# Kernel optimization log

Measured on AMD Instinct MI355X. Metric: run time of the kernel, lower is better.

The kernel has to match this reference:

```python
import jax, jax.numpy as jnp
from jax import lax
import numpy as np

C = 64
K = 3  # kernel_size
PAD = K // 2


def setup_inputs() -> dict:
    key = jax.random.key(0)
    k1, k2, k3, k4, k5 = jax.random.split(key, 5)
    B, N, H, W = 2, 16, 96, 96
    x = jax.random.normal(k1, (B, C, N, H, W), dtype=jnp.float32)
    # offset conv: Conv2d(C, 2K, kernel=(1,K)) -> 1D conv weight (2K, C, K)
    w_off = jax.random.normal(k2, (2 * K, C, K), dtype=jnp.float32) * 0.05
    b_off = jax.random.normal(k3, (2 * K,), dtype=jnp.float32) * 0.05
    # deform conv: DeformConv2d(C, C, kernel=(1,K)) -> weight (C, C, K)
    w_def = jax.random.normal(k4, (C, C, K), dtype=jnp.float32) * (1.0 / np.sqrt(C * K))
    b_def = jax.random.normal(k5, (C,), dtype=jnp.float32) * 0.01
    return {"x": x, "w_off": w_off, "b_off": b_off, "w_def": w_def, "b_def": b_def}


def _deform_fuse(x, w_off, b_off, w_def, b_def):
    B, Cc, N, H, W = x.shape
    M = B * H * W
    # (B,C,N,H,W) -> (B,H,W,C,N) -> (M, C, N); the 'width' axis is the focus axis N
    xm = jnp.transpose(x, (0, 3, 4, 1, 2)).reshape(M, Cc, N)

    # offset-predicting 1D conv over N, padding K//2 (same)
    offsets = lax.conv_general_dilated(
        xm, w_off, window_strides=(1,), padding=[(PAD, PAD)],
        dimension_numbers=("NCH", "OIH", "NCH"),
    ) + b_off[None, :, None]  # (M, 2K, N)
    # torchvision ordering: per kernel tap j, channel 2j = dy, 2j+1 = dx
    off_y = offsets[:, 0::2]  # (M, K, N)
    off_x = offsets[:, 1::2]  # (M, K, N)

    # base sampling positions along the (width=N) axis: n - pad + j
    pos = (jnp.arange(N, dtype=x.dtype)[None, :] - PAD
           + jnp.arange(K, dtype=x.dtype)[:, None])  # (K, N)
    px = pos[None] + off_x                            # (M, K, N)
    x0 = jnp.floor(px)
    fx = px - x0                                      # fractional part
    x0i = x0.astype(jnp.int32)
    x1i = x0i + 1
    v0 = ((x0i >= 0) & (x0i < N)).astype(x.dtype)
    v1 = ((x1i >= 0) & (x1i < N)).astype(x.dtype)
    c0 = jnp.clip(x0i, 0, N - 1)
    c1 = jnp.clip(x1i, 0, N - 1)

    # gather along N per row: (C,N) indexed by (K,N) -> (C,K,N)
    gather = jax.vmap(lambda xr, idx: xr[:, idx])
    g0 = gather(xm, c0) * (v0 * (1.0 - fx))[:, None]   # (M, C, K, N)
    g1 = gather(xm, c1) * (v1 * fx)[:, None]
    # height dim is size 1: bilinear weight along y collapses to relu(1-|dy|)
    wy = jnp.maximum(jnp.array(0.0, x.dtype), 1.0 - jnp.abs(off_y))[:, None]  # (M,1,K,N)
    val = (g0 + g1) * wy                               # (M, C, K, N)

    out = jnp.einsum("ock,mckn->mon", w_def, val) + b_def[None, :, None]  # (M, C, N)
    out = out.reshape(B, H, W, Cc, N)
    return jnp.transpose(out, (0, 3, 4, 1, 2))         # (B, C, N, H, W)


def reference(x, w_off, b_off, w_def, b_def):
    return _deform_fuse(x, w_off, b_off, w_def, b_def)
```

## Files before the change

### kernel.cpp

```cpp
#include <hip/hip_runtime.h>
#include <stdint.h>


typedef __attribute__((ext_vector_type(8))) short short8;
typedef __attribute__((ext_vector_type(4))) float f32x4;

#define XT_OFF   0
#define XST_OFF  20480
#define PB       36864
#define A0_OFF   (PB)
#define A1_OFF   (PB + 1536)
#define R0_OFF   (PB + 3072)
#define OFFS_OFF (PB + 4608)
#define LDS_BYTES (PB + 7680)

__device__ __forceinline__ short f2bf(float f) {
  union { float f; uint32_t u; } v; v.f = f;
  uint32_t r = (v.u + 0x7FFFu + ((v.u >> 16) & 1u)) >> 16;
  return (short)r;
}
__device__ __forceinline__ float bf2f(short s) {
  union { uint32_t u; float f; } v; v.u = ((uint32_t)(uint16_t)s) << 16; return v.f;
}

__global__ __launch_bounds__(256) void prep_kernel(
    const float* __restrict__ w_off, const float* __restrict__ w_def, short8* __restrict__ ws)
{
  int gid = blockIdx.x * 256 + threadIdx.x;
  if (gid < 1536) {
    int mt = gid / 384, ks = (gid % 384) >> 6, ll = gid & 63;
    int m = mt * 16 + (ll & 15), rgq = ll >> 4;
    short8 v;
    #pragma unroll
    for (int jj = 0; jj < 8; ++jj) {
      int kk = ks * 32 + rgq * 8 + jj;
      int c = kk & 63, k3 = kk >> 6;
      v[jj] = f2bf(w_def[m * 192 + c * 3 + k3]);
    }
    ws[gid] = v;
  } else if (gid < 1920) {
    int q = gid - 1536;
    int ks = q >> 6, ll = q & 63;
    int m = ll & 15, rgq = ll >> 4;
    short8 v;
    #pragma unroll
    for (int jj = 0; jj < 8; ++jj) {
      int kk = ks * 32 + rgq * 8 + jj;
      int c = kk & 63, k3 = kk >> 6;
      v[jj] = (m < 6) ? f2bf(w_off[m * 192 + c * 3 + k3]) : (short)0;
    }
    ws[gid] = v;
  }
}

__global__ __launch_bounds__(256, 3) void deform_main(
    const float* __restrict__ x, const float* __restrict__ b_off,
    const float* __restrict__ b_def, const short8* __restrict__ wfr,
    float* __restrict__ out)
{
  extern __shared__ char smem[];
  const int t = threadIdx.x, wv = t >> 6, l = t & 63, col = l & 15, rg = l >> 4;
  const int tn = blockIdx.x;
  const int wt = tn % 12, bh = tn / 12;
  const int h = bh % 96, b = bh / 96, w0 = wt * 8;
  const float* xb = x + (size_t)b * 9437184 + h * 96 + w0;

  uint16_t* xst = (uint16_t*)(smem + XST_OFF);
  #pragma unroll
  for (int i = 0; i < 8; ++i) {
    int r = (t >> 1) + i * 128, half = t & 1;
    float4 v = *(const float4*)(xb + (size_t)r * 9216 + half * 4);
    uint32_t p0 = (uint32_t)(uint16_t)f2bf(v.x) | ((uint32_t)(uint16_t)f2bf(v.y) << 16);
    uint32_t p1 = (uint32_t)(uint16_t)f2bf(v.z) | ((uint32_t)(uint16_t)f2bf(v.w) << 16);
    uint2 pk; pk.x = p0; pk.y = p1;
    *(uint2*)(xst + r * 8 + half * 4) = pk;
  }
  __syncthreads();

  #pragma unroll
  for (int i = 0; i < 4; ++i) {
    int item = t + 256 * i;
    int pos = item & 127, cg = item >> 7;
    short8 v;
    #pragma unroll
    for (int jj = 0; jj < 8; ++jj) v[jj] = (short)xst[(cg * 8 + jj) * 128 + pos];
    *(short8*)(smem + XT_OFF + pos * 160 + cg * 16) = v;
  }
  __syncthreads();

  float* offs = (float*)(smem + OFFS_OFF);
  {
    f32x4 cacc[2] = {{0.f,0.f,0.f,0.f},{0.f,0.f,0.f,0.f}};
    const short8 zero = {0,0,0,0,0,0,0,0};
    for (int ks = 0; ks < 6; ++ks) {
      short8 av = wfr[1536 + ks * 64 + l];
      int k3 = ks >> 1;
      #pragma unroll
      for (int nt2 = 0; nt2 < 2; ++nt2) {
        int pos = (wv * 2 + nt2) * 16 + col;
        int n = pos >> 3, w = pos & 7;
        int row = n + k3 - 1;
        bool valid = (row >= 0) && (row < 16);
        int rcl = min(max(row, 0), 15);
        short8 bv = *(short8*)(smem + XT_OFF + (rcl * 8 + w) * 160 + rg * 16 + (ks & 1) * 64);
        bv = valid ? bv : zero;
        cacc[nt2] = __builtin_amdgcn_mfma_f32_16x16x32_bf16(av, bv, cacc[nt2], 0, 0, 0);
      }
    }
    #pragma unroll
    for (int nt2 = 0; nt2 < 2; ++nt2) {
      int pos = (wv * 2 + nt2) * 16 + col;
      #pragma unroll
      for (int r = 0; r < 4; ++r) {
        int rowo = rg * 4 + r;
        if (rowo < 6) offs[rowo * 128 + pos] = cacc[nt2][r];
      }
    }
  }
  __syncthreads();

  float* A0 = (float*)(smem + A0_OFF);
  float* A1 = (float*)(smem + A1_OFF);
  int*   R0 = (int*)(smem + R0_OFF);
  for (int it = t; it < 384; it += 256) {
    int k = it >> 7, pos = it & 127;
    int n = pos >> 3, w = pos & 7;
    float oy = offs[(2 * k) * 128 + pos] + b_off[2 * k];
    float ox = offs[(2 * k + 1) * 128 + pos] + b_off[2 * k + 1];
    float px = (float)(n - 1 + k) + ox;
    float x0f = floorf(px);
    float fx = px - x0f;
    int x0 = (int)x0f;
    float wy = fmaxf(0.f, 1.f - fabsf(oy));
    float wt1v = fx * wy;
    float wt0v = wy - wt1v;
    float a0, a1; int r0;
    if (x0 >= 0 && x0 < 15)  { r0 = x0; a0 = wt0v; a1 = wt1v; }
    else if (x0 == 15)       { r0 = 14; a0 = 0.f;  a1 = wt0v; }
    else if (x0 == -1)       { r0 = 0;  a0 = wt1v; a1 = 0.f;  }
    else                     { r0 = 0;  a0 = 0.f;  a1 = 0.f;  }
    A0[it] = a0; A1[it] = a1;
    R0[it] = (r0 * 8 + w) * 160;
  }
  __syncthreads();

  f32x4 acc[4][2];
  #pragma unroll
  for (int mt = 0; mt < 4; ++mt) {
    float4 bd = *(const float4*)(b_def + mt * 16 + rg * 4);
    #pragma unroll
    for (int nt2 = 0; nt2 < 2; ++nt2) {
      acc[mt][nt2][0] = bd.x; acc[mt][nt2][1] = bd.y;
      acc[mt][nt2][2] = bd.z; acc[mt][nt2][3] = bd.w;
    }
  }
  #pragma unroll 1
  for (int k3 = 0; k3 < 3; ++k3) {
    float a0v[2], a1v[2]; int rb[2];
    #pragma unroll
    for (int nt2 = 0; nt2 < 2; ++nt2) {
      int idx = k3 * 128 + (wv * 2 + nt2) * 16 + col;
      a0v[nt2] = A0[idx]; a1v[nt2] = A1[idx]; rb[nt2] = R0[idx];
    }
    #pragma unroll
    for (int ks2 = 0; ks2 < 2; ++ks2) {
      int ks = k3 * 2 + ks2;
      short8 A[4];
      #pragma unroll
      for (int mt = 0; mt < 4; ++mt) A[mt] = wfr[(mt * 6 + ks) * 64 + l];
      #pragma unroll
      for (int nt2 = 0; nt2 < 2; ++nt2) {
        const char* base = smem + XT_OFF + rb[nt2] + rg * 16 + ks2 * 64;
        short8 x0 = *(const short8*)base;
        short8 x1 = *(const short8*)(base + 1280);
        short8 bv;
        #pragma unroll
        for (int jj = 0; jj < 8; ++jj)
          bv[jj] = f2bf(a0v[nt2] * bf2f(x0[jj]) + a1v[nt2] * bf2f(x1[jj]));
        #pragma unroll
        for (int mt = 0; mt < 4; ++mt)
          acc[mt][nt2] = __builtin_amdgcn_mfma_f32_16x16x32_bf16(A[mt], bv, acc[mt][nt2], 0, 0, 0);
      }
    }
  }
  __syncthreads();

  float* stg = (float*)(smem + XT_OFF);
  #pragma unroll
  for (int mt = 0; mt < 4; ++mt) {
    #pragma unroll
    for (int nt2 = 0; nt2 < 2; ++nt2) {
      int pos = (wv * 2 + nt2) * 16 + col;
      #pragma unroll
      for (int r = 0; r < 4; ++r) {
        int o = mt * 16 + rg * 4 + r;
        stg[o * 132 + pos] = acc[mt][nt2][r];
      }
    }
  }
  __syncthreads();
  float* ob = out + (size_t)b * 9437184 + h * 96 + w0;
  for (int s2 = t; s2 < 2048; s2 += 256) {
    int q = s2 >> 1, half = s2 & 1;
    int o = q >> 4, n = q & 15;
    float4 v = *(float4*)(stg + o * 132 + n * 8 + half * 4);
    *(float4*)(ob + (size_t)(o * 16 + n) * 9216 + half * 4) = v;
  }
}

extern "C" void kernel_launch(void* const* d_in, const int* in_sizes, int n_in,
                              void* d_out, int out_size, void* d_ws, size_t ws_size,
                              hipStream_t stream) {
  (void)in_sizes; (void)n_in; (void)ws_size; (void)out_size;
  const float* x     = (const float*)d_in[0];
  const float* w_off = (const float*)d_in[1];
  const float* b_off = (const float*)d_in[2];
  const float* w_def = (const float*)d_in[3];
  const float* b_def = (const float*)d_in[4];
  float* out = (float*)d_out;
  short8* wfr = (short8*)d_ws;

  prep_kernel<<<dim3(8), dim3(256), 0, stream>>>(w_off, w_def, wfr);
  deform_main<<<dim3(2304), dim3(256), LDS_BYTES, stream>>>(x, b_off, b_def, wfr, out);
}
```

Before: 205.4 us.

## Make deform kernel persistent over three tiles with register prefetch of next tile

The grid shrinks from 2304 to 768 blocks, and each block now loops over three tiles. The next tile's x data is prefetched into registers while the current tile is computed, which is meant to hide global load latency. A block-index swizzle reorders tiles. Bilinear coefficients are now computed per thread in registers instead of through LDS arrays with an extra barrier, and biases are loaded once per block. The cost is higher register pressure from the 8 float4 prefetch buffers, which may reduce occupancy under launch_bounds(256,3). Fewer blocks also means less parallelism for latency hiding.

```diff
diff --git a/kernel.cpp b/kernel.cpp
--- a/kernel.cpp
+++ b/kernel.cpp
@@ -7,12 +7,8 @@
 
 #define XT_OFF   0
 #define XST_OFF  20480
-#define PB       36864
-#define A0_OFF   (PB)
-#define A1_OFF   (PB + 1536)
-#define R0_OFF   (PB + 3072)
-#define OFFS_OFF (PB + 4608)
-#define LDS_BYTES (PB + 7680)
+#define OFFS_OFF 36864
+#define LDS_BYTES 39936
 
 __device__ __forceinline__ short f2bf(float f) {
   union { float f; uint32_t u; } v; v.f = f;
@@ -59,152 +55,184 @@
     float* __restrict__ out)
 {
   extern __shared__ char smem[];
+  uint16_t* xst = (uint16_t*)(smem + XST_OFF);
+  float* offs = (float*)(smem + OFFS_OFF);
+  float* stg  = (float*)(smem + XT_OFF);
+
   const int t = threadIdx.x, wv = t >> 6, l = t & 63, col = l & 15, rg = l >> 4;
-  const int tn = blockIdx.x;
-  const int wt = tn % 12, bh = tn / 12;
-  const int h = bh % 96, b = bh / 96, w0 = wt * 8;
-  const float* xb = x + (size_t)b * 9437184 + h * 96 + w0;
-
-  uint16_t* xst = (uint16_t*)(smem + XST_OFF);
+  const int p = blockIdx.x;
+  const int swz = (p & ~15) | ((p & 7) << 1) | ((p >> 3) & 1);
+
+  float bo[6];
   #pragma unroll
-  for (int i = 0; i < 8; ++i) {
-    int r = (t >> 1) + i * 128, half = t & 1;
-    float4 v = *(const float4*)(xb + (size_t)r * 9216 + half * 4);
-    uint32_t p0 = (uint32_t)(uint16_t)f2bf(v.x) | ((uint32_t)(uint16_t)f2bf(v.y) << 16);
-    uint32_t p1 = (uint32_t)(uint16_t)f2bf(v.z) | ((uint32_t)(uint16_t)f2bf(v.w) << 16);
-    uint2 pk; pk.x = p0; pk.y = p1;
-    *(uint2*)(xst + r * 8 + half * 4) = pk;
+  for (int i = 0; i < 6; ++i) bo[i] = b_off[i];
+  float4 bdv[4];
+  #pragma unroll
+  for (int mt = 0; mt < 4; ++mt) bdv[mt] = *(const float4*)(b_def + mt * 16 + rg * 4);
+
+  float4 xr[8];
+  {
+    int tn = swz;
+    int wt = tn % 12, bh = tn / 12, h = bh % 96, b = bh / 96;
+    const float* xb = x + (size_t)b * 9437184 + h * 96 + wt * 8;
+    #pragma unroll
+    for (int i = 0; i < 8; ++i) {
+      int r = (t >> 1) + i * 128;
+      xr[i] = *(const float4*)(xb + (size_t)r * 9216 + (t & 1) * 4);
+    }
   }
-  __syncthreads();
-
-  #pragma unroll
-  for (int i = 0; i < 4; ++i) {
-    int item = t + 256 * i;
-    int pos = item & 127, cg = item >> 7;
-    short8 v;
-    #pragma unroll
-    for (int jj = 0; jj < 8; ++jj) v[jj] = (short)xst[(cg * 8 + jj) * 128 + pos];
-    *(short8*)(smem + XT_OFF + pos * 160 + cg * 16) = v;
-  }
-  __syncthreads();
-
-  float* offs = (float*)(smem + OFFS_OFF);
-  {
-    f32x4 cacc[2] = {{0.f,0.f,0.f,0.f},{0.f,0.f,0.f,0.f}};
-    const short8 zero = {0,0,0,0,0,0,0,0};
-    for (int ks = 0; ks < 6; ++ks) {
-      short8 av = wfr[1536 + ks * 64 + l];
-      int k3 = ks >> 1;
+
+  for (int j = 0; j < 3; ++j) {
+    const int tn = swz + 768 * j;
+    const int wt = tn % 12, bh = tn / 12, h = bh % 96, b = bh / 96;
+    const int w0 = wt * 8;
+
+    __syncthreads();
+
+    #pragma unroll
+    for (int i = 0; i < 8; ++i) {
+      int r = (t >> 1) + i * 128, half = t & 1;
+      float4 v = xr[i];
+      uint32_t p0 = (uint32_t)(uint16_t)f2bf(v.x) | ((uint32_t)(uint16_t)f2bf(v.y) << 16);
+      uint32_t p1 = (uint32_t)(uint16_t)f2bf(v.z) | ((uint32_t)(uint16_t)f2bf(v.w) << 16);
+      uint2 pk; pk.x = p0; pk.y = p1;
+      *(uint2*)(xst + r * 8 + half * 4) = pk;
+    }
+
+    if (j < 2) {
+      int tn2 = tn + 768;
+      int wt2 = tn2 % 12, bh2 = tn2 / 12, h2 = bh2 % 96, b2 = bh2 / 96;
+      const float* xb2 = x + (size_t)b2 * 9437184 + h2 * 96 + wt2 * 8;
+      #pragma unroll
+      for (int i = 0; i < 8; ++i) {
+        int r = (t >> 1) + i * 128;
+        xr[i] = *(const float4*)(xb2 + (size_t)r * 9216 + (t & 1) * 4);
+      }
+    }
+    __syncthreads();
+
+    #pragma unroll
+    for (int i = 0; i < 4; ++i) {
+      int item = t + 256 * i;
+      int pos = item & 127, cg = item >> 7;
+      short8 v;
+      #pragma unroll
+      for (int jj = 0; jj < 8; ++jj) v[jj] = (short)xst[(cg * 8 + jj) * 128 + pos];
+      *(short8*)(smem + XT_OFF + pos * 160 + cg * 16) = v;
+    }
+    __syncthreads();
+
+    {
+      f32x4 cacc[2] = {{0.f,0.f,0.f,0.f},{0.f,0.f,0.f,0.f}};
+      const short8 zero = {0,0,0,0,0,0,0,0};
+      for (int ks = 0; ks < 6; ++ks) {
+        short8 av = wfr[1536 + ks * 64 + l];
+        int k3 = ks >> 1;
+        #pragma unroll
+        for (int nt2 = 0; nt2 < 2; ++nt2) {
+          int pos = (wv * 2 + nt2) * 16 + col;
+          int n = pos >> 3, w = pos & 7;
+          int row = n + k3 - 1;
+          bool valid = (row >= 0) && (row < 16);
+          int rcl = min(max(row, 0), 15);
+          short8 bv = *(short8*)(smem + XT_OFF + (rcl * 8 + w) * 160 + rg * 16 + (ks & 1) * 64);
+          bv = valid ? bv : zero;
+          cacc[nt2] = __builtin_amdgcn_mfma_f32_16x16x32_bf16(av, bv, cacc[nt2], 0, 0, 0);
+        }
+      }
+      #pragma unroll
+      for (int nt2 = 0; nt2 < 2; ++nt2) {
+        int pos = (wv * 2 + nt2) * 16 + col;
+        #pragma unroll
+        for (int r = 0; r < 4; ++r) {
+          int rowo = rg * 4 + r;
+          if (rowo < 6) offs[rowo * 128 + pos] = cacc[nt2][r];
+        }
+      }
+    }
+
+    float a0v[3][2], a1v[3][2]; int rb[3][2];
+    #pragma unroll
+    for (int k = 0; k < 3; ++k) {
       #pragma unroll
       for (int nt2 = 0; nt2 < 2; ++nt2) {
         int pos = (wv * 2 + nt2) * 16 + col;
         int n = pos >> 3, w = pos & 7;
-        int row = n + k3 - 1;
-        bool valid = (row >= 0) && (row < 16);
-        int rcl = min(max(row, 0), 15);
-        short8 bv = *(short8*)(smem + XT_OFF + (rcl * 8 + w) * 160 + rg * 16 + (ks & 1) * 64);
-        bv = valid ? bv : zero;
-        cacc[nt2] = __builtin_amdgcn_mfma_f32_16x16x32_bf16(av, bv, cacc[nt2], 0, 0, 0);
-      }
-    }
-    #pragma unroll
-    for (int nt2 = 0; nt2 < 2; ++nt2) {
-      int pos = (wv * 2 + nt2) * 16 + col;
-      #pragma unroll
-      for (int r = 0; r < 4; ++r) {
-        int rowo = rg * 4 + r;
-        if (rowo < 6) offs[rowo * 128 + pos] = cacc[nt2][r];
-      }
-    }
-  }
-  __syncthreads();
-
-  float* A0 = (float*)(smem + A0_OFF);
-  float* A1 = (float*)(smem + A1_OFF);
-  int*   R0 = (int*)(smem + R0_OFF);
-  for (int it = t; it < 384; it += 256) {
-    int k = it >> 7, pos = it & 127;
-    int n = pos >> 3, w = pos & 7;
-    float oy = offs[(2 * k) * 128 + pos] + b_off[2 * k];
-    float ox = offs[(2 * k + 1) * 128 + pos] + b_off[2 * k + 1];
-    float px = (float)(n - 1 + k) + ox;
-    float x0f = floorf(px);
-    float fx = px - x0f;
-    int x0 = (int)x0f;
-    float wy = fmaxf(0.f, 1.f - fabsf(oy));
-    float wt1v = fx * wy;
-    float wt0v = wy - wt1v;
-    float a0, a1; int r0;
-    if (x0 >= 0 && x0 < 15)  { r0 = x0; a0 = wt0v; a1 = wt1v; }
-    else if (x0 == 15)       { r0 = 14; a0 = 0.f;  a1 = wt0v; }
-    else if (x0 == -1)       { r0 = 0;  a0 = wt1v; a1 = 0.f;  }
-    else                     { r0 = 0;  a0 = 0.f;  a1 = 0.f;  }
-    A0[it] = a0; A1[it] = a1;
-    R0[it] = (r0 * 8 + w) * 160;
-  }
-  __syncthreads();
-
-  f32x4 acc[4][2];
-  #pragma unroll
-  for (int mt = 0; mt < 4; ++mt) {
-    float4 bd = *(const float4*)(b_def + mt * 16 + rg * 4);
-    #pragma unroll
-    for (int nt2 = 0; nt2 < 2; ++nt2) {
-      acc[mt][nt2][0] = bd.x; acc[mt][nt2][1] = bd.y;
-      acc[mt][nt2][2] = bd.z; acc[mt][nt2][3] = bd.w;
-    }
-  }
-  #pragma unroll 1
-  for (int k3 = 0; k3 < 3; ++k3) {
-    float a0v[2], a1v[2]; int rb[2];
-    #pragma unroll
-    for (int nt2 = 0; nt2 < 2; ++nt2) {
-      int idx = k3 * 128 + (wv * 2 + nt2) * 16 + col;
-      a0v[nt2] = A0[idx]; a1v[nt2] = A1[idx]; rb[nt2] = R0[idx];
-    }
-    #pragma unroll
-    for (int ks2 = 0; ks2 < 2; ++ks2) {
-      int ks = k3 * 2 + ks2;
-      short8 A[4];
-      #pragma unroll
-      for (int mt = 0; mt < 4; ++mt) A[mt] = wfr[(mt * 6 + ks) * 64 + l];
-      #pragma unroll
-      for (int nt2 = 0; nt2 < 2; ++nt2) {
-        const char* base = smem + XT_OFF + rb[nt2] + rg * 16 + ks2 * 64;
-        short8 x0 = *(const short8*)base;
-        short8 x1 = *(const short8*)(base + 1280);
-        short8 bv;
-        #pragma unroll
-        for (int jj = 0; jj < 8; ++jj)
-          bv[jj] = f2bf(a0v[nt2] * bf2f(x0[jj]) + a1v[nt2] * bf2f(x1[jj]));
-        #pragma unroll
-        for (int mt = 0; mt < 4; ++mt)
-          acc[mt][nt2] = __builtin_amdgcn_mfma_f32_16x16x32_bf16(A[mt], bv, acc[mt][nt2], 0, 0, 0);
-      }
-    }
-  }
-  __syncthreads();
-
-  float* stg = (float*)(smem + XT_OFF);
-  #pragma unroll
-  for (int mt = 0; mt < 4; ++mt) {
-    #pragma unroll
-    for (int nt2 = 0; nt2 < 2; ++nt2) {
-      int pos = (wv * 2 + nt2) * 16 + col;
-      #pragma unroll
-      for (int r = 0; r < 4; ++r) {
-        int o = mt * 16 + rg * 4 + r;
-        stg[o * 132 + pos] = acc[mt][nt2][r];
-      }
-    }
-  }
-  __syncthreads();
-  float* ob = out + (size_t)b * 9437184 + h * 96 + w0;
-  for (int s2 = t; s2 < 2048; s2 += 256) {
-    int q = s2 >> 1, half = s2 & 1;
-    int o = q >> 4, n = q & 15;
-    float4 v = *(float4*)(stg + o * 132 + n * 8 + half * 4);
-    *(float4*)(ob + (size_t)(o * 16 + n) * 9216 + half * 4) = v;
+        float oy = offs[(2 * k) * 128 + pos] + bo[2 * k];
+        float ox = offs[(2 * k + 1) * 128 + pos] + bo[2 * k + 1];
+        float px = (float)(n - 1 + k) + ox;
+        float x0f = floorf(px);
+        float fx = px - x0f;
+        int x0 = (int)x0f;
+        float wy = fmaxf(0.f, 1.f - fabsf(oy));
+        float wt1v = fx * wy;
+        float wt0v = wy - wt1v;
+        float a0, a1; int r0;
+        if (x0 >= 0 && x0 < 15)  { r0 = x0; a0 = wt0v; a1 = wt1v; }
+        else if (x0 == 15)       { r0 = 14; a0 = 0.f;  a1 = wt0v; }
+        else if (x0 == -1)       { r0 = 0;  a0 = wt1v; a1 = 0.f;  }
+        else                     { r0 = 0;  a0 = 0.f;  a1 = 0.f;  }
+        a0v[k][nt2] = a0; a1v[k][nt2] = a1;
+        rb[k][nt2] = (r0 * 8 + w) * 160;
+      }
+    }
+
+    f32x4 acc[4][2];
+    #pragma unroll
+    for (int mt = 0; mt < 4; ++mt) {
+      #pragma unroll
+      for (int nt2 = 0; nt2 < 2; ++nt2) {
+        acc[mt][nt2][0] = bdv[mt].x; acc[mt][nt2][1] = bdv[mt].y;
+        acc[mt][nt2][2] = bdv[mt].z; acc[mt][nt2][3] = bdv[mt].w;
+      }
+    }
+    #pragma unroll 1
+    for (int k3 = 0; k3 < 3; ++k3) {
+      #pragma unroll
+      for (int ks2 = 0; ks2 < 2; ++ks2) {
+        int ks = k3 * 2 + ks2;
+        short8 A[4];
+        #pragma unroll
+        for (int mt = 0; mt < 4; ++mt) A[mt] = wfr[(mt * 6 + ks) * 64 + l];
+        #pragma unroll
+        for (int nt2 = 0; nt2 < 2; ++nt2) {
+          const char* base = smem + XT_OFF + rb[k3][nt2] + rg * 16 + ks2 * 64;
+          short8 x0 = *(const short8*)base;
+          short8 x1 = *(const short8*)(base + 1280);
+          short8 bv;
+          #pragma unroll
+          for (int jj = 0; jj < 8; ++jj)
+            bv[jj] = f2bf(a0v[k3][nt2] * bf2f(x0[jj]) + a1v[k3][nt2] * bf2f(x1[jj]));
+          #pragma unroll
+          for (int mt = 0; mt < 4; ++mt)
+            acc[mt][nt2] = __builtin_amdgcn_mfma_f32_16x16x32_bf16(A[mt], bv, acc[mt][nt2], 0, 0, 0);
+        }
+      }
+    }
+    __syncthreads();
+
+    #pragma unroll
+    for (int mt = 0; mt < 4; ++mt) {
+      #pragma unroll
+      for (int nt2 = 0; nt2 < 2; ++nt2) {
+        int pos = (wv * 2 + nt2) * 16 + col;
+        #pragma unroll
+        for (int r = 0; r < 4; ++r) {
+          int o = mt * 16 + rg * 4 + r;
+          stg[o * 132 + pos] = acc[mt][nt2][r];
+        }
+      }
+    }
+    __syncthreads();
+    float* ob = out + (size_t)b * 9437184 + h * 96 + w0;
+    #pragma unroll
+    for (int i = 0; i < 8; ++i) {
+      int s2 = t + 256 * i;
+      int q = s2 >> 1, half = s2 & 1;
+      int o = q >> 4, n = q & 15;
+      float4 v = *(float4*)(stg + o * 132 + n * 8 + half * 4);
+      *(float4*)(ob + (size_t)(o * 16 + n) * 9216 + half * 4) = v;
+    }
   }
 }
 
@@ -221,5 +249,5 @@
   short8* wfr = (short8*)d_ws;
 
   prep_kernel<<<dim3(8), dim3(256), 0, stream>>>(w_off, w_def, wfr);
-  deform_main<<<dim3(2304), dim3(256), LDS_BYTES, stream>>>(x, b_off, b_def, wfr, out);
-}
+  deform_main<<<dim3(768), dim3(256), LDS_BYTES, stream>>>(x, b_off, b_def, wfr, out);
+}
```

Result: slower. 228.6 us (+11.3%).

## Shrink LDS footprint, compute sampling weights in registers, remap block order

Applied to the files above, without the earlier changes.

Shrinks the LDS layout: the transposed tile row stride drops from 160 to 144 bytes, and the staging and offset buffers alias one region. Total LDS falls from about 44.5KB to 34KB, and launch bounds now request 4 blocks per CU instead of 3. The per-position bilinear weights and row bases are now computed directly in each thread's registers instead of staged through LDS, which removes a sync and the LDS round trip. Block indices are permuted so adjacent blocks pair differently, aiming for better cache locality. The risks are higher register pressure from fully unrolled loops and a new LDS bank-conflict pattern from the 144-byte stride.

```diff
diff --git a/kernel.cpp b/kernel.cpp
--- a/kernel.cpp
+++ b/kernel.cpp
@@ -6,13 +6,9 @@
 typedef __attribute__((ext_vector_type(4))) float f32x4;
 
 #define XT_OFF   0
-#define XST_OFF  20480
-#define PB       36864
-#define A0_OFF   (PB)
-#define A1_OFF   (PB + 1536)
-#define R0_OFF   (PB + 3072)
-#define OFFS_OFF (PB + 4608)
-#define LDS_BYTES (PB + 7680)
+#define XG_OFF   18432
+#define OFFS_OFF 18432
+#define LDS_BYTES 34816
 
 __device__ __forceinline__ short f2bf(float f) {
   union { float f; uint32_t u; } v; v.f = f;
@@ -53,19 +49,23 @@
   }
 }
 
-__global__ __launch_bounds__(256, 3) void deform_main(
+__global__ __launch_bounds__(256, 4) void deform_main(
     const float* __restrict__ x, const float* __restrict__ b_off,
     const float* __restrict__ b_def, const short8* __restrict__ wfr,
     float* __restrict__ out)
 {
   extern __shared__ char smem[];
+  uint16_t* xst = (uint16_t*)(smem + XG_OFF);
+  float* offs   = (float*)(smem + OFFS_OFF);
+  float* stg    = (float*)(smem + XT_OFF);
+
   const int t = threadIdx.x, wv = t >> 6, l = t & 63, col = l & 15, rg = l >> 4;
-  const int tn = blockIdx.x;
+  const int p = blockIdx.x;
+  const int tn = (p & ~15) | ((p & 7) << 1) | ((p >> 3) & 1);
   const int wt = tn % 12, bh = tn / 12;
   const int h = bh % 96, b = bh / 96, w0 = wt * 8;
   const float* xb = x + (size_t)b * 9437184 + h * 96 + w0;
 
-  uint16_t* xst = (uint16_t*)(smem + XST_OFF);
   #pragma unroll
   for (int i = 0; i < 8; ++i) {
     int r = (t >> 1) + i * 128, half = t & 1;
@@ -84,14 +84,14 @@
     short8 v;
     #pragma unroll
     for (int jj = 0; jj < 8; ++jj) v[jj] = (short)xst[(cg * 8 + jj) * 128 + pos];
-    *(short8*)(smem + XT_OFF + pos * 160 + cg * 16) = v;
-  }
-  __syncthreads();
-
-  float* offs = (float*)(smem + OFFS_OFF);
+    *(short8*)(smem + XT_OFF + pos * 144 + cg * 16) = v;
+  }
+  __syncthreads();
+
   {
     f32x4 cacc[2] = {{0.f,0.f,0.f,0.f},{0.f,0.f,0.f,0.f}};
     const short8 zero = {0,0,0,0,0,0,0,0};
+    #pragma unroll
     for (int ks = 0; ks < 6; ++ks) {
       short8 av = wfr[1536 + ks * 64 + l];
       int k3 = ks >> 1;
@@ -102,7 +102,7 @@
         int row = n + k3 - 1;
         bool valid = (row >= 0) && (row < 16);
         int rcl = min(max(row, 0), 15);
-        short8 bv = *(short8*)(smem + XT_OFF + (rcl * 8 + w) * 160 + rg * 16 + (ks & 1) * 64);
+        short8 bv = *(short8*)(smem + XT_OFF + (rcl * 8 + w) * 144 + rg * 16 + (ks & 1) * 64);
         bv = valid ? bv : zero;
         cacc[nt2] = __builtin_amdgcn_mfma_f32_16x16x32_bf16(av, bv, cacc[nt2], 0, 0, 0);
       }
@@ -117,32 +117,32 @@
       }
     }
   }
-  __syncthreads();
-
-  float* A0 = (float*)(smem + A0_OFF);
-  float* A1 = (float*)(smem + A1_OFF);
-  int*   R0 = (int*)(smem + R0_OFF);
-  for (int it = t; it < 384; it += 256) {
-    int k = it >> 7, pos = it & 127;
-    int n = pos >> 3, w = pos & 7;
-    float oy = offs[(2 * k) * 128 + pos] + b_off[2 * k];
-    float ox = offs[(2 * k + 1) * 128 + pos] + b_off[2 * k + 1];
-    float px = (float)(n - 1 + k) + ox;
-    float x0f = floorf(px);
-    float fx = px - x0f;
-    int x0 = (int)x0f;
-    float wy = fmaxf(0.f, 1.f - fabsf(oy));
-    float wt1v = fx * wy;
-    float wt0v = wy - wt1v;
-    float a0, a1; int r0;
-    if (x0 >= 0 && x0 < 15)  { r0 = x0; a0 = wt0v; a1 = wt1v; }
-    else if (x0 == 15)       { r0 = 14; a0 = 0.f;  a1 = wt0v; }
-    else if (x0 == -1)       { r0 = 0;  a0 = wt1v; a1 = 0.f;  }
-    else                     { r0 = 0;  a0 = 0.f;  a1 = 0.f;  }
-    A0[it] = a0; A1[it] = a1;
-    R0[it] = (r0 * 8 + w) * 160;
-  }
-  __syncthreads();
+
+  float a0v[3][2], a1v[3][2]; int rb[3][2];
+  #pragma unroll
+  for (int k = 0; k < 3; ++k) {
+    #pragma unroll
+    for (int nt2 = 0; nt2 < 2; ++nt2) {
+      int pos = (wv * 2 + nt2) * 16 + col;
+      int n = pos >> 3, w = pos & 7;
+      float oy = offs[(2 * k) * 128 + pos] + b_off[2 * k];
+      float ox = offs[(2 * k + 1) * 128 + pos] + b_off[2 * k + 1];
+      float px = (float)(n - 1 + k) + ox;
+      float x0f = floorf(px);
+      float fx = px - x0f;
+      int x0 = (int)x0f;
+      float wy = fmaxf(0.f, 1.f - fabsf(oy));
+      float wt1v = fx * wy;
+      float wt0v = wy - wt1v;
+      float a0, a1; int r0;
+      if (x0 >= 0 && x0 < 15)  { r0 = x0; a0 = wt0v; a1 = wt1v; }
+      else if (x0 == 15)       { r0 = 14; a0 = 0.f;  a1 = wt0v; }
+      else if (x0 == -1)       { r0 = 0;  a0 = wt1v; a1 = 0.f;  }
+      else                     { r0 = 0;  a0 = 0.f;  a1 = 0.f;  }
+      a0v[k][nt2] = a0; a1v[k][nt2] = a1;
+      rb[k][nt2] = (r0 * 8 + w) * 144;
+    }
+  }
 
   f32x4 acc[4][2];
   #pragma unroll
@@ -154,14 +154,8 @@
       acc[mt][nt2][2] = bd.z; acc[mt][nt2][3] = bd.w;
     }
   }
-  #pragma unroll 1
+  #pragma unroll
   for (int k3 = 0; k3 < 3; ++k3) {
-    float a0v[2], a1v[2]; int rb[2];
-    #pragma unroll
-    for (int nt2 = 0; nt2 < 2; ++nt2) {
-      int idx = k3 * 128 + (wv * 2 + nt2) * 16 + col;
-      a0v[nt2] = A0[idx]; a1v[nt2] = A1[idx]; rb[nt2] = R0[idx];
-    }
     #pragma unroll
     for (int ks2 = 0; ks2 < 2; ++ks2) {
       int ks = k3 * 2 + ks2;
@@ -170,13 +164,13 @@
       for (int mt = 0; mt < 4; ++mt) A[mt] = wfr[(mt * 6 + ks) * 64 + l];
       #pragma unroll
       for (int nt2 = 0; nt2 < 2; ++nt2) {
-        const char* base = smem + XT_OFF + rb[nt2] + rg * 16 + ks2 * 64;
+        const char* base = smem + XT_OFF + rb[k3][nt2] + rg * 16 + ks2 * 64;
         short8 x0 = *(const short8*)base;
-        short8 x1 = *(const short8*)(base + 1280);
+        short8 x1 = *(const short8*)(base + 1152);
         short8 bv;
         #pragma unroll
         for (int jj = 0; jj < 8; ++jj)
-          bv[jj] = f2bf(a0v[nt2] * bf2f(x0[jj]) + a1v[nt2] * bf2f(x1[jj]));
+          bv[jj] = f2bf(a0v[k3][nt2] * bf2f(x0[jj]) + a1v[k3][nt2] * bf2f(x1[jj]));
         #pragma unroll
         for (int mt = 0; mt < 4; ++mt)
           acc[mt][nt2] = __builtin_amdgcn_mfma_f32_16x16x32_bf16(A[mt], bv, acc[mt][nt2], 0, 0, 0);
@@ -185,7 +179,6 @@
   }
   __syncthreads();
 
-  float* stg = (float*)(smem + XT_OFF);
   #pragma unroll
   for (int mt = 0; mt < 4; ++mt) {
     #pragma unroll
@@ -200,7 +193,9 @@
   }
   __syncthreads();
   float* ob = out + (size_t)b * 9437184 + h * 96 + w0;
-  for (int s2 = t; s2 < 2048; s2 += 256) {
+  #pragma unroll
+  for (int i = 0; i < 8; ++i) {
+    int s2 = t + 256 * i;
     int q = s2 >> 1, half = s2 & 1;
     int o = q >> 4, n = q & 15;
     float4 v = *(float4*)(stg + o * 132 + n * 8 + half * 4);
@@ -220,6 +215,8 @@
   float* out = (float*)d_out;
   short8* wfr = (short8*)d_ws;
 
+  (void)hipFuncSetAttribute((const void*)deform_main,
+                            hipFuncAttributeMaxDynamicSharedMemorySize, LDS_BYTES);
   prep_kernel<<<dim3(8), dim3(256), 0, stream>>>(w_off, w_def, wfr);
   deform_main<<<dim3(2304), dim3(256), LDS_BYTES, stream>>>(x, b_off, b_def, wfr, out);
 }
```

After: 182.7 us. -11.1%, faster.
